# Kernel optimization log

Measured on AMD Instinct MI355X. Metric: run time of the kernel, lower is better.

The kernel has to match this reference:

```python
import jax, jax.numpy as jnp
import numpy as np

B, S, D, H = 2, 2048, 1024, 16
DK = D // H

def setup_inputs() -> dict:
    key = jax.random.key(0)
    ks = jax.random.split(key, 12)
    sc = 1.0 / np.sqrt(D)
    inp = {
        'query': jax.random.normal(ks[0], (B, S, D), jnp.float32),
        'key':   jax.random.normal(ks[1], (B, S, D), jnp.float32),
        'value': jax.random.normal(ks[2], (B, S, D), jnp.float32),
        'attn_mask': jnp.tril(jnp.ones((S, S), jnp.int32))[None, None],  # [1,1,S,S] causal
        'Wq': jax.random.normal(ks[3], (D, D), jnp.float32) * sc,
        'bq': jnp.zeros((D,), jnp.float32),
        'Wk': jax.random.normal(ks[4], (D, D), jnp.float32) * sc,
        'bk': jnp.zeros((D,), jnp.float32),
        'Wv': jax.random.normal(ks[5], (D, D), jnp.float32) * sc,
        'bv': jnp.zeros((D,), jnp.float32),
        'Wo': jax.random.normal(ks[6], (D, D), jnp.float32) * sc,
        'bo': jnp.zeros((D,), jnp.float32),
    }
    return inp

def reference(query, key, value, attn_mask, Wq, bq, Wk, bk, Wv, bv, Wo, bo):
    # QKV projections, split heads: [B,S,D] -> [B,H,S,DK]
    def proj(x, W, b):
        y = jnp.einsum('bsd,ed->bse', x, W) + b  # torch Linear: x @ W.T + b
        return y.reshape(B, S, H, DK).transpose(0, 2, 1, 3)
    q, k, v = proj(query, Wq, bq), proj(key, Wk, bk), proj(value, Wv, bv)
    scores = jnp.einsum('bhqd,bhkd->bhqk', q, k) / jnp.sqrt(jnp.float32(DK))
    scores = jnp.where(attn_mask == 0, jnp.float32(-1e9), scores)
    p_attn = jax.nn.softmax(scores, axis=-1)  # dropout = identity (eval)
    attn_outputs = jnp.einsum('bhqk,bhkd->bhqd', p_attn, v)  # [B,H,S,DK]
    # NOTE: module's quirk: 'attn_weights' is mean over d_k of the attended values
    attn_weights = jnp.mean(attn_outputs, axis=-1)  # [B,H,S]
    out = attn_outputs.transpose(0, 2, 1, 3).reshape(B, S, D)
    out = jnp.einsum('bsd,ed->bse', out, Wo) + bo
    return (out, attn_weights)
```

## Files before the change

kernel.cpp:

```cpp
#include <hip/hip_runtime.h>
#include <hip/hip_bf16.h>
#include <stdint.h>

#define B_ 2
#define S_ 2048
#define D_ 1024
#define H_ 16
#define DK_ 64
#define M_ 4096
#define K_ 1024

typedef unsigned short u16;
typedef u16   u16x4  __attribute__((ext_vector_type(4)));
typedef short short8 __attribute__((ext_vector_type(8)));
typedef float f32x4  __attribute__((ext_vector_type(4)));
typedef uint32_t u32x4 __attribute__((ext_vector_type(4)));

__device__ __forceinline__ u16 f2bf(float f) {
  uint32_t u = __builtin_bit_cast(uint32_t, f);
  u += 0x7FFFu + ((u >> 16) & 1u);
  return (u16)(u >> 16);
}

__device__ __forceinline__ uint32_t cvtpk(float lo, float hi) {
  uint32_t r;
  asm("v_cvt_pk_bf16_f32 %0, %1, %2" : "=v"(r) : "v"(lo), "v"(hi));
  return r;
}

__device__ __forceinline__ void gload_lds16(const void* g, void* l) {
  __builtin_amdgcn_global_load_lds(
      (const __attribute__((address_space(1))) void*)g,
      (__attribute__((address_space(3))) void*)l, 16, 0, 0);
}

__global__ __launch_bounds__(256) void cvt4w(const float* __restrict__ a,
                                             const float* __restrict__ b,
                                             const float* __restrict__ c,
                                             const float* __restrict__ d,
                                             u16* __restrict__ oa, u16* __restrict__ ob,
                                             u16* __restrict__ oc, u16* __restrict__ od) {
  const int z = blockIdx.y;
  const float* in = z == 0 ? a : (z == 1 ? b : (z == 2 ? c : d));
  u16* out = z == 0 ? oa : (z == 1 ? ob : (z == 2 ? oc : od));
  const int i = (blockIdx.x * 256 + threadIdx.x) * 4;
  const float4 v = *(const float4*)(in + i);
  u16x4 o;
  o[0] = f2bf(v.x); o[1] = f2bf(v.y); o[2] = f2bf(v.z); o[3] = f2bf(v.w);
  *(u16x4*)(out + i) = o;
}

__global__ __launch_bounds__(256) void gemm_qkv(
    const float* __restrict__ Aq, const float* __restrict__ Ak, const float* __restrict__ Av,
    const u16* __restrict__ Wqp, const u16* __restrict__ Wkp, const u16* __restrict__ Wvp,
    const float* __restrict__ bqp, const float* __restrict__ bkp, const float* __restrict__ bvp,
    u16* __restrict__ oq, u16* __restrict__ okk, u16* __restrict__ ov) {
  __shared__ float As[2][128 * 32];
  __shared__ u16  Bs[2][128 * 32];

  const int g = blockIdx.x;
  const int T = (g & 7) * 96 + (g >> 3);
  const int z = T >> 8;
  const int rem = T & 255;
  const int m0 = (rem >> 3) * 128, n0 = (rem & 7) * 128;

  const float* A    = z == 0 ? Aq  : (z == 1 ? Ak  : Av);
  const u16*   W    = z == 0 ? Wqp : (z == 1 ? Wkp : Wvp);
  const float* bias = z == 0 ? bqp : (z == 1 ? bkp : bvp);
  u16* out          = z == 0 ? oq  : (z == 1 ? okk : ov);
  const float scale = z == 0 ? 0.125f : 1.0f;

  const int tid = threadIdx.x;
  const int w = tid >> 6, lane = tid & 63;
  const int lr = lane & 15, lk = lane >> 4;
  const int wr = w >> 1, wc = w & 1;

  f32x4 acc[4][4] = {};

  const int arow   = tid >> 3;
  const int acolsz = ((tid & 7) * 16) ^ ((arow & 7) << 4);
  const int brow   = tid >> 2;
  const int bcolsz = ((tid & 3) * 16) ^ ((brow & 3) << 4);
  const int raswz  = (lr & 7) << 4;
  const int rbswz  = (lr & 3) << 4;
  const float* Ab = A + (size_t)(m0 + arow) * K_;
  const u16*   Wb = W + (size_t)(n0 + brow) * K_;

  auto STAGE = [&](int k0, int d) {
#pragma unroll
    for (int i = 0; i < 4; ++i)
      gload_lds16((const char*)(Ab + (size_t)(i * 32) * K_ + k0) + acolsz,
                  (char*)As[d] + i * 4096 + w * 1024);
#pragma unroll
    for (int i = 0; i < 2; ++i)
      gload_lds16((const char*)(Wb + (size_t)(i * 64) * K_ + k0) + bcolsz,
                  (char*)Bs[d] + i * 4096 + w * 1024);
  };

  STAGE(0, 0);
  __syncthreads();

  int cur = 0;
  for (int t = 0; t < 32; ++t) {
    if (t + 1 < 32) STAGE((t + 1) * 32, cur ^ 1);

    short8 af[4], bf[4];
#pragma unroll
    for (int mi = 0; mi < 4; ++mi) {
      const char* ap = (const char*)As[cur] + (wr * 64 + mi * 16 + lr) * 128;
      const f32x4 lo = *(const f32x4*)(ap + ((lk * 32) ^ raswz));
      const f32x4 hi = *(const f32x4*)(ap + ((lk * 32 + 16) ^ raswz));
      u32x4 pk;
      pk[0] = cvtpk(lo[0], lo[1]);
      pk[1] = cvtpk(lo[2], lo[3]);
      pk[2] = cvtpk(hi[0], hi[1]);
      pk[3] = cvtpk(hi[2], hi[3]);
      af[mi] = __builtin_bit_cast(short8, pk);
    }
#pragma unroll
    for (int nj = 0; nj < 4; ++nj)
      bf[nj] = *(const short8*)((const char*)Bs[cur] + (wc * 64 + nj * 16 + lr) * 64 +
                                ((lk * 16) ^ rbswz));
#pragma unroll
    for (int mi = 0; mi < 4; ++mi)
#pragma unroll
      for (int nj = 0; nj < 4; ++nj)
        acc[mi][nj] = __builtin_amdgcn_mfma_f32_16x16x32_bf16(af[mi], bf[nj],
                                                              acc[mi][nj], 0, 0, 0);
    __syncthreads();
    cur ^= 1;
  }

#pragma unroll
  for (int nj = 0; nj < 4; ++nj) {
    const int col = n0 + wc * 64 + nj * 16 + lr;
    const float bv = bias[col];
    const int h = col >> 6, dk = col & 63;
#pragma unroll
    for (int mi = 0; mi < 4; ++mi) {
#pragma unroll
      for (int r = 0; r < 4; ++r) {
        const int row = m0 + wr * 64 + mi * 16 + lk * 4 + r;
        const float val = (acc[mi][nj][r] + bv) * scale;
        const int b = row >> 11, s = row & 2047;
        if (z != 2)
          out[((size_t)(b * H_ + h) * S_ + s) * DK_ + dk] = f2bf(val);
        else
          out[((size_t)(b * H_ + h) * DK_ + dk) * S_ + s] = f2bf(val);
      }
    }
  }
}

__global__ __launch_bounds__(256) void gemm_out(const u16* __restrict__ A,
                                                const u16* __restrict__ W,
                                                const float* __restrict__ bias,
                                                float* __restrict__ out) {
  __shared__ u16 As[2][128 * 32];
  __shared__ u16 Bs[2][128 * 32];
  const int g = blockIdx.x;
  const int T = (g & 7) * 32 + (g >> 3);
  const int m0 = (T >> 3) * 128, n0 = (T & 7) * 128;

  const int tid = threadIdx.x;
  const int w = tid >> 6, lane = tid & 63;
  const int lr = lane & 15, lk = lane >> 4;
  const int wr = w >> 1, wc = w & 1;

  f32x4 acc[4][4] = {};

  const int brow   = tid >> 2;
  const int bcolsz = ((tid & 3) * 16) ^ ((brow & 3) << 4);
  const int rbswz  = (lr & 3) << 4;
  const u16* Abase = A + (size_t)(m0 + brow) * K_;
  const u16* Wbase = W + (size_t)(n0 + brow) * K_;

  auto STAGE = [&](int k0, int d) {
#pragma unroll
    for (int i = 0; i < 2; ++i) {
      gload_lds16((const char*)(Abase + (size_t)(i * 64) * K_ + k0) + bcolsz,
                  (char*)As[d] + i * 4096 + w * 1024);
      gload_lds16((const char*)(Wbase + (size_t)(i * 64) * K_ + k0) + bcolsz,
                  (char*)Bs[d] + i * 4096 + w * 1024);
    }
  };

  STAGE(0, 0);
  __syncthreads();

  int cur = 0;
  for (int t = 0; t < 32; ++t) {
    if (t + 1 < 32) STAGE((t + 1) * 32, cur ^ 1);

    short8 af[4], bf[4];
#pragma unroll
    for (int mi = 0; mi < 4; ++mi)
      af[mi] = *(const short8*)((const char*)As[cur] + (wr * 64 + mi * 16 + lr) * 64 +
                                ((lk * 16) ^ rbswz));
#pragma unroll
    for (int nj = 0; nj < 4; ++nj)
      bf[nj] = *(const short8*)((const char*)Bs[cur] + (wc * 64 + nj * 16 + lr) * 64 +
                                ((lk * 16) ^ rbswz));
#pragma unroll
    for (int mi = 0; mi < 4; ++mi)
#pragma unroll
      for (int nj = 0; nj < 4; ++nj)
        acc[mi][nj] = __builtin_amdgcn_mfma_f32_16x16x32_bf16(af[mi], bf[nj],
                                                              acc[mi][nj], 0, 0, 0);
    __syncthreads();
    cur ^= 1;
  }

#pragma unroll
  for (int nj = 0; nj < 4; ++nj) {
    const int col = n0 + wc * 64 + nj * 16 + lr;
    const float bv = bias[col];
#pragma unroll
    for (int mi = 0; mi < 4; ++mi)
#pragma unroll
      for (int r = 0; r < 4; ++r) {
        const int row = m0 + wr * 64 + mi * 16 + lk * 4 + r;
        out[(size_t)row * D_ + col] = acc[mi][nj][r] + bv;
      }
  }
}

__global__ __launch_bounds__(256) void flash64(const u16* __restrict__ Qh,
                                               const u16* __restrict__ Kh,
                                               const u16* __restrict__ Vt,
                                               u16* __restrict__ O,
                                               float* __restrict__ AW) {
  __shared__ u16 Ks[2][64 * 64];
  __shared__ u16 Vs[2][64 * 64];
  __shared__ u16 Ps[64 * 64];
  const int tid = threadIdx.x;
  const int w = tid >> 6, lane = tid & 63;
  const int lr = lane & 15, lk = lane >> 4;
  const int bh = blockIdx.x;
  const int qt = (gridDim.y - 1) - blockIdx.y;
  const int q0 = qt * 64;
  const int b = bh >> 4, h = bh & 15;
  const int nt = qt + 1;

  const u16* Qg = Qh + ((size_t)bh * S_ + q0 + w * 16 + lr) * DK_;
  short8 qf[2];
  qf[0] = *(const short8*)(Qg + lk * 8);
  qf[1] = *(const short8*)(Qg + 32 + lk * 8);

  float mrow[4], lrow[4];
  f32x4 o[4] = {};
#pragma unroll
  for (int r = 0; r < 4; ++r) { mrow[r] = -__builtin_inff(); lrow[r] = 0.f; }

  const int trow = tid >> 3;
  const int tswz = ((tid & 7) * 16) ^ ((trow & 7) << 4);
  const int rswz = (lr & 7) << 4;
  const u16* Kgb = Kh + (size_t)bh * S_ * DK_;
  const u16* Vgb = Vt + (size_t)bh * DK_ * S_;

  auto STAGE = [&](int t, int d) {
    const int kv0 = t * 64;
#pragma unroll
    for (int i = 0; i < 2; ++i) {
      const char* gk = (const char*)(Kgb + (size_t)(kv0 + i * 32 + trow) * DK_) + tswz;
      gload_lds16(gk, (char*)Ks[d] + i * 4096 + w * 1024);
      const char* gv = (const char*)(Vgb + (size_t)(i * 32 + trow) * S_ + kv0) + tswz;
      gload_lds16(gv, (char*)Vs[d] + i * 4096 + w * 1024);
    }
  };

  STAGE(0, 0);
  __syncthreads();

  int cur = 0;
  for (int t = 0; t < nt; ++t) {
    if (t + 1 < nt) STAGE(t + 1, cur ^ 1);

    f32x4 sa[4] = {};
#pragma unroll
    for (int kk = 0; kk < 2; ++kk)
#pragma unroll
      for (int nj = 0; nj < 4; ++nj) {
        const short8 kf = *(const short8*)((const char*)Ks[cur] + (nj * 16 + lr) * 128 +
                                           ((kk * 64 + lk * 16) ^ rswz));
        sa[nj] = __builtin_amdgcn_mfma_f32_16x16x32_bf16(qf[kk], kf, sa[nj], 0, 0, 0);
      }

    if (t == qt) {
#pragma unroll
      for (int nj = 0; nj < 4; ++nj)
#pragma unroll
        for (int r = 0; r < 4; ++r)
          if (nj * 16 + lr > w * 16 + lk * 4 + r) sa[nj][r] = -1e30f;
    }

#pragma unroll
    for (int r = 0; r < 4; ++r) {
      float mx = fmaxf(fmaxf(sa[0][r], sa[1][r]), fmaxf(sa[2][r], sa[3][r]));
#pragma unroll
      for (int d = 1; d < 16; d <<= 1) mx = fmaxf(mx, __shfl_xor(mx, d));
      const float mn = fmaxf(mrow[r], mx);
      const float sc = __expf(mrow[r] - mn);
      mrow[r] = mn;
      float rs = 0.f;
#pragma unroll
      for (int nj = 0; nj < 4; ++nj) {
        const float p = __expf(sa[nj][r] - mn);
        sa[nj][r] = p;
        rs += p;
      }
      lrow[r] = lrow[r] * sc + rs;
#pragma unroll
      for (int nj = 0; nj < 4; ++nj) o[nj][r] *= sc;
    }

#pragma unroll
    for (int nj = 0; nj < 4; ++nj)
#pragma unroll
      for (int r = 0; r < 4; ++r) {
        const int rp = w * 16 + lk * 4 + r;
        *(u16*)((char*)Ps + rp * 128 + (((nj * 16 + lr) * 2) ^ ((rp & 7) << 4))) =
            f2bf(sa[nj][r]);
      }

#pragma unroll
    for (int kk = 0; kk < 2; ++kk) {
      const short8 pa = *(const short8*)((const char*)Ps + (w * 16 + lr) * 128 +
                                         ((kk * 64 + lk * 16) ^ rswz));
#pragma unroll
      for (int nj = 0; nj < 4; ++nj) {
        const short8 vf = *(const short8*)((const char*)Vs[cur] + (nj * 16 + lr) * 128 +
                                           ((kk * 64 + lk * 16) ^ rswz));
        o[nj] = __builtin_amdgcn_mfma_f32_16x16x32_bf16(pa, vf, o[nj], 0, 0, 0);
      }
    }
    __syncthreads();
    cur ^= 1;
  }

#pragma unroll
  for (int r = 0; r < 4; ++r) {
    float lt = lrow[r];
#pragma unroll
    for (int d = 1; d < 16; d <<= 1) lt += __shfl_xor(lt, d);
    const int rowq = q0 + w * 16 + lk * 4 + r;
    const float inv = 1.f / lt;
    float rsum = 0.f;
#pragma unroll
    for (int nj = 0; nj < 4; ++nj) {
      const float v = o[nj][r] * inv;
      O[((size_t)(b * S_ + rowq)) * D_ + h * 64 + nj * 16 + lr] = f2bf(v);
      rsum += v;
    }
#pragma unroll
    for (int d = 1; d < 16; d <<= 1) rsum += __shfl_xor(rsum, d);
    if (lr == 0) AW[(size_t)bh * S_ + rowq] = rsum * (1.f / 64.f);
  }
}

extern "C" void kernel_launch(void* const* d_in, const int* in_sizes, int n_in,
                              void* d_out, int out_size, void* d_ws, size_t ws_size,
                              hipStream_t stream) {
  const float* q  = (const float*)d_in[0];
  const float* k  = (const float*)d_in[1];
  const float* v  = (const float*)d_in[2];
  const float* Wq = (const float*)d_in[4];
  const float* bq = (const float*)d_in[5];
  const float* Wk = (const float*)d_in[6];
  const float* bk = (const float*)d_in[7];
  const float* Wv = (const float*)d_in[8];
  const float* bv = (const float*)d_in[9];
  const float* Wo = (const float*)d_in[10];
  const float* bo = (const float*)d_in[11];
  float* out = (float*)d_out;
  float* aw  = out + (size_t)M_ * D_;

  char* ws = (char*)d_ws;
  u16* Qh  = (u16*)(ws);
  u16* Kh  = (u16*)(ws + (8u << 20));
  u16* Vtb = (u16*)(ws + (16u << 20));
  u16* Ob  = (u16*)(ws + (24u << 20));
  u16* Wqb = (u16*)(ws + (32u << 20));
  u16* Wkb = (u16*)(ws + (34u << 20));
  u16* Wvb = (u16*)(ws + (36u << 20));
  u16* Wob = (u16*)(ws + (38u << 20));

  cvt4w<<<dim3(1024, 4), 256, 0, stream>>>(Wq, Wk, Wv, Wo, Wqb, Wkb, Wvb, Wob);

  gemm_qkv<<<768, 256, 0, stream>>>(q, k, v, Wqb, Wkb, Wvb,
                                    bq, bk, bv, Qh, Kh, Vtb);

  flash64<<<dim3(B_ * H_, S_ / 64), 256, 0, stream>>>(Qh, Kh, Vtb, Ob, aw);

  gemm_out<<<256, 256, 0, stream>>>(Ob, Wob, bo, out);
}
```

Baseline: 272.0 us.

## Triple-buffer GEMM k-loops and convert A to bf16 before the LDS stage

Both projection GEMMs move from a double-buffered loop with __syncthreads to a three-stage LDS ring with explicit vmcnt waits and raw s_barrier, keeping two tiles of loads in flight behind the MFMA work. In the QKV GEMM, the fp32 activations are now loaded into registers, packed to bf16 once, and written to LDS as bf16. This halves A's LDS footprint and removes the per-wave repeated conversions at fragment-read time. In exchange there are more registers for the prefetched tiles, more LDS for the third buffer, and a hand-counted waitcnt schedule that must stay correct.

```diff
diff --git a/kernel.cpp b/kernel.cpp
--- a/kernel.cpp
+++ b/kernel.cpp
@@ -33,6 +33,11 @@
       (const __attribute__((address_space(1))) void*)g,
       (__attribute__((address_space(3))) void*)l, 16, 0, 0);
 }
+
+#define WAITV(N) do { asm volatile("s_waitcnt vmcnt(" #N ")" ::: "memory"); \
+                      __builtin_amdgcn_sched_barrier(0); } while (0)
+#define WAITL0   do { asm volatile("s_waitcnt lgkmcnt(0)" ::: "memory"); \
+                      __builtin_amdgcn_sched_barrier(0); } while (0)
 
 __global__ __launch_bounds__(256) void cvt4w(const float* __restrict__ a,
                                              const float* __restrict__ b,
@@ -55,8 +60,8 @@
     const u16* __restrict__ Wqp, const u16* __restrict__ Wkp, const u16* __restrict__ Wvp,
     const float* __restrict__ bqp, const float* __restrict__ bkp, const float* __restrict__ bvp,
     u16* __restrict__ oq, u16* __restrict__ okk, u16* __restrict__ ov) {
-  __shared__ float As[2][128 * 32];
-  __shared__ u16  Bs[2][128 * 32];
+  __shared__ u16 As[3][128 * 32];
+  __shared__ u16 Bs[3][128 * 32];
 
   const int g = blockIdx.x;
   const int T = (g & 7) * 96 + (g >> 3);
@@ -77,58 +82,75 @@
 
   f32x4 acc[4][4] = {};
 
-  const int arow   = tid >> 3;
-  const int acolsz = ((tid & 7) * 16) ^ ((arow & 7) << 4);
+  const int s_row  = tid >> 1;
+  const int s_half = tid & 1;
+  const int wswz   = (s_row & 3) << 4;
+  const float* Agl = A + (size_t)(m0 + s_row) * K_ + s_half * 16;
   const int brow   = tid >> 2;
   const int bcolsz = ((tid & 3) * 16) ^ ((brow & 3) << 4);
-  const int raswz  = (lr & 7) << 4;
-  const int rbswz  = (lr & 3) << 4;
-  const float* Ab = A + (size_t)(m0 + arow) * K_;
-  const u16*   Wb = W + (size_t)(n0 + brow) * K_;
-
-  auto STAGE = [&](int k0, int d) {
-#pragma unroll
-    for (int i = 0; i < 4; ++i)
-      gload_lds16((const char*)(Ab + (size_t)(i * 32) * K_ + k0) + acolsz,
-                  (char*)As[d] + i * 4096 + w * 1024);
+  const u16* Wb    = W + (size_t)(n0 + brow) * K_;
+  const int rswz   = (lr & 3) << 4;
+
+  f32x4 ra[4], rb[4];
+
+  auto LOADA = [&](int t, f32x4 (&r)[4]) {
+    const f32x4* p = (const f32x4*)(Agl + t * 32);
+#pragma unroll
+    for (int i = 0; i < 4; ++i) r[i] = p[i];
+  };
+  auto BLD = [&](int t, int buf) {
 #pragma unroll
     for (int i = 0; i < 2; ++i)
-      gload_lds16((const char*)(Wb + (size_t)(i * 64) * K_ + k0) + bcolsz,
-                  (char*)Bs[d] + i * 4096 + w * 1024);
-  };
-
-  STAGE(0, 0);
-  __syncthreads();
-
-  int cur = 0;
-  for (int t = 0; t < 32; ++t) {
-    if (t + 1 < 32) STAGE((t + 1) * 32, cur ^ 1);
-
+      gload_lds16((const char*)(Wb + (size_t)(i * 64) * K_ + t * 32) + bcolsz,
+                  (char*)Bs[buf] + i * 4096 + w * 1024);
+  };
+  auto WRITEA = [&](const f32x4 (&r)[4], int buf) {
+    u32x4 w0, w1;
+    w0[0] = cvtpk(r[0][0], r[0][1]); w0[1] = cvtpk(r[0][2], r[0][3]);
+    w0[2] = cvtpk(r[1][0], r[1][1]); w0[3] = cvtpk(r[1][2], r[1][3]);
+    w1[0] = cvtpk(r[2][0], r[2][1]); w1[1] = cvtpk(r[2][2], r[2][3]);
+    w1[2] = cvtpk(r[3][0], r[3][1]); w1[3] = cvtpk(r[3][2], r[3][3]);
+    char* base = (char*)As[buf] + s_row * 64;
+    *(u32x4*)(base + ((s_half * 32) ^ wswz))      = w0;
+    *(u32x4*)(base + ((s_half * 32 + 16) ^ wswz)) = w1;
+  };
+  auto COMPUTE = [&](int buf) {
     short8 af[4], bf[4];
 #pragma unroll
-    for (int mi = 0; mi < 4; ++mi) {
-      const char* ap = (const char*)As[cur] + (wr * 64 + mi * 16 + lr) * 128;
-      const f32x4 lo = *(const f32x4*)(ap + ((lk * 32) ^ raswz));
-      const f32x4 hi = *(const f32x4*)(ap + ((lk * 32 + 16) ^ raswz));
-      u32x4 pk;
-      pk[0] = cvtpk(lo[0], lo[1]);
-      pk[1] = cvtpk(lo[2], lo[3]);
-      pk[2] = cvtpk(hi[0], hi[1]);
-      pk[3] = cvtpk(hi[2], hi[3]);
-      af[mi] = __builtin_bit_cast(short8, pk);
-    }
+    for (int mi = 0; mi < 4; ++mi)
+      af[mi] = *(const short8*)((const char*)As[buf] + (wr * 64 + mi * 16 + lr) * 64 +
+                                ((lk * 16) ^ rswz));
 #pragma unroll
     for (int nj = 0; nj < 4; ++nj)
-      bf[nj] = *(const short8*)((const char*)Bs[cur] + (wc * 64 + nj * 16 + lr) * 64 +
-                                ((lk * 16) ^ rbswz));
+      bf[nj] = *(const short8*)((const char*)Bs[buf] + (wc * 64 + nj * 16 + lr) * 64 +
+                                ((lk * 16) ^ rswz));
 #pragma unroll
     for (int mi = 0; mi < 4; ++mi)
 #pragma unroll
       for (int nj = 0; nj < 4; ++nj)
         acc[mi][nj] = __builtin_amdgcn_mfma_f32_16x16x32_bf16(af[mi], bf[nj],
                                                               acc[mi][nj], 0, 0, 0);
-    __syncthreads();
-    cur ^= 1;
+  };
+
+  LOADA(0, ra); BLD(0, 0);
+  LOADA(1, rb); BLD(1, 1);
+  WAITV(6);
+  WRITEA(ra, 0);
+  WAITL0;
+  __builtin_amdgcn_s_barrier();
+
+  for (int t = 0; t < 32; t += 2) {
+    if (t + 2 < 32) { LOADA(t + 2, ra); BLD(t + 2, (t + 2) % 3); }
+    COMPUTE(t % 3);
+    if (t + 2 < 32) WAITV(6); else WAITV(0);
+    WRITEA(rb, (t + 1) % 3);
+    WAITL0;
+    __builtin_amdgcn_s_barrier();
+    if (t + 3 < 32) { LOADA(t + 3, rb); BLD(t + 3, (t + 3) % 3); }
+    COMPUTE((t + 1) % 3);
+    if (t + 3 < 32) { WAITV(6); } else { WAITV(0); }
+    if (t + 2 < 32) { WRITEA(ra, (t + 2) % 3); WAITL0; }
+    __builtin_amdgcn_s_barrier();
   }
 
 #pragma unroll
@@ -156,8 +178,8 @@
                                                 const u16* __restrict__ W,
                                                 const float* __restrict__ bias,
                                                 float* __restrict__ out) {
-  __shared__ u16 As[2][128 * 32];
-  __shared__ u16 Bs[2][128 * 32];
+  __shared__ u16 As[3][128 * 32];
+  __shared__ u16 Bs[3][128 * 32];
   const int g = blockIdx.x;
   const int T = (g & 7) * 32 + (g >> 3);
   const int m0 = (T >> 3) * 128, n0 = (T & 7) * 128;
@@ -171,44 +193,46 @@
 
   const int brow   = tid >> 2;
   const int bcolsz = ((tid & 3) * 16) ^ ((brow & 3) << 4);
-  const int rbswz  = (lr & 3) << 4;
-  const u16* Abase = A + (size_t)(m0 + brow) * K_;
-  const u16* Wbase = W + (size_t)(n0 + brow) * K_;
-
-  auto STAGE = [&](int k0, int d) {
+  const int rswz   = (lr & 3) << 4;
+  const u16* Ab = A + (size_t)(m0 + brow) * K_;
+  const u16* Wb = W + (size_t)(n0 + brow) * K_;
+
+  auto STAGE = [&](int t, int buf) {
 #pragma unroll
     for (int i = 0; i < 2; ++i) {
-      gload_lds16((const char*)(Abase + (size_t)(i * 64) * K_ + k0) + bcolsz,
-                  (char*)As[d] + i * 4096 + w * 1024);
-      gload_lds16((const char*)(Wbase + (size_t)(i * 64) * K_ + k0) + bcolsz,
-                  (char*)Bs[d] + i * 4096 + w * 1024);
-    }
-  };
-
-  STAGE(0, 0);
-  __syncthreads();
-
-  int cur = 0;
-  for (int t = 0; t < 32; ++t) {
-    if (t + 1 < 32) STAGE((t + 1) * 32, cur ^ 1);
-
+      gload_lds16((const char*)(Ab + (size_t)(i * 64) * K_ + t * 32) + bcolsz,
+                  (char*)As[buf] + i * 4096 + w * 1024);
+      gload_lds16((const char*)(Wb + (size_t)(i * 64) * K_ + t * 32) + bcolsz,
+                  (char*)Bs[buf] + i * 4096 + w * 1024);
+    }
+  };
+  auto COMPUTE = [&](int buf) {
     short8 af[4], bf[4];
 #pragma unroll
     for (int mi = 0; mi < 4; ++mi)
-      af[mi] = *(const short8*)((const char*)As[cur] + (wr * 64 + mi * 16 + lr) * 64 +
-                                ((lk * 16) ^ rbswz));
+      af[mi] = *(const short8*)((const char*)As[buf] + (wr * 64 + mi * 16 + lr) * 64 +
+                                ((lk * 16) ^ rswz));
 #pragma unroll
     for (int nj = 0; nj < 4; ++nj)
-      bf[nj] = *(const short8*)((const char*)Bs[cur] + (wc * 64 + nj * 16 + lr) * 64 +
-                                ((lk * 16) ^ rbswz));
+      bf[nj] = *(const short8*)((const char*)Bs[buf] + (wc * 64 + nj * 16 + lr) * 64 +
+                                ((lk * 16) ^ rswz));
 #pragma unroll
     for (int mi = 0; mi < 4; ++mi)
 #pragma unroll
       for (int nj = 0; nj < 4; ++nj)
         acc[mi][nj] = __builtin_amdgcn_mfma_f32_16x16x32_bf16(af[mi], bf[nj],
                                                               acc[mi][nj], 0, 0, 0);
-    __syncthreads();
-    cur ^= 1;
+  };
+
+  STAGE(0, 0); STAGE(1, 1);
+  WAITV(4);
+  __builtin_amdgcn_s_barrier();
+
+  for (int t = 0; t < 32; ++t) {
+    if (t + 2 < 32) STAGE(t + 2, (t + 2) % 3);
+    COMPUTE(t % 3);
+    if (t + 2 < 32) WAITV(4); else WAITV(0);
+    __builtin_amdgcn_s_barrier();
   }
 
 #pragma unroll
```

After: 280.7 us. 3.2% more time.
